# Kernel tuning notes

Measured on AMD Instinct MI355X. Metric: run time of the kernel, lower is better.

The kernel has to match this reference:

```python
import jax, jax.numpy as jnp
import numpy as np

N = 50000        # nodes
E = 800000       # directed edges (before self-loops)
HID = 128
HEADS = 4
LAYERS = 4
D = HID // HEADS  # per-head dim = 32
NEG_SLOPE = 0.2
EPS = 1e-5


def setup_inputs() -> dict:
    key = jax.random.key(0)
    ks = jax.random.split(key, 12)
    s = 0.1
    x = jax.random.normal(ks[0], (N, HID), jnp.float32)
    edge_index = jax.random.randint(ks[1], (2, E), 0, N, jnp.int32)
    # GATv2Conv params per layer: lin_l (source), lin_r (target), att vector, bias
    Wl = s * jax.random.normal(ks[2], (LAYERS, HID, HID), jnp.float32)
    Wr = s * jax.random.normal(ks[3], (LAYERS, HID, HID), jnp.float32)
    att = s * jax.random.normal(ks[4], (LAYERS, HEADS, D), jnp.float32)
    conv_b = jnp.zeros((LAYERS, HID), jnp.float32)
    # GraphNorm params
    gn_w = jnp.ones((LAYERS, HID), jnp.float32)
    gn_b = jnp.zeros((LAYERS, HID), jnp.float32)
    gn_ms = jnp.ones((LAYERS, HID), jnp.float32)  # mean_scale
    # skip projection + final fc
    skip_W = s * jax.random.normal(ks[5], (HID, HID), jnp.float32)
    skip_b = jnp.zeros((HID,), jnp.float32)
    fc_W = s * jax.random.normal(ks[6], (HID, 1), jnp.float32)
    fc_b = jnp.zeros((1,), jnp.float32)
    return {"x": x, "edge_index": edge_index, "Wl": Wl, "Wr": Wr, "att": att,
            "conv_b": conv_b, "gn_w": gn_w, "gn_b": gn_b, "gn_ms": gn_ms,
            "skip_W": skip_W, "skip_b": skip_b, "fc_W": fc_W, "fc_b": fc_b}


def _gatv2_layer(x, src, dst, Wl, Wr, att, bias, n):
    # GATv2Conv: x_l = W_l x_j (messages), x_r = W_r x_i (targets)
    xl = (x @ Wl).reshape(n, HEADS, D)
    xr = (x @ Wr).reshape(n, HEADS, D)
    # edge-wise attention logits: a^T LeakyReLU(x_l[j] + x_r[i])
    e = jax.nn.leaky_relu(xl[src] + xr[dst], NEG_SLOPE)      # [E, H, D]
    score = jnp.einsum('ehd,hd->eh', e, att)                 # [E, H]
    # scatter-softmax over incoming edges of each target node
    smax = jax.ops.segment_max(score, dst, num_segments=n)   # [N, H]
    a = jnp.exp(score - smax[dst])
    denom = jax.ops.segment_sum(a, dst, num_segments=n)
    alpha = a / denom[dst]                                   # [E, H]
    out = jax.ops.segment_sum(alpha[:, :, None] * xl[src], dst, num_segments=n)
    return out.reshape(n, HID) + bias


def _graph_norm(h, w, b, ms):
    # single-graph GraphNorm: x - mean_scale*mean, scaled by per-channel std
    mean = h.mean(axis=0)
    hc = h - ms * mean
    var = (hc * hc).mean(axis=0)
    return w * hc / jnp.sqrt(var + EPS) + b


def reference(x, edge_index, Wl, Wr, att, conv_b, gn_w, gn_b, gn_ms,
              skip_W, skip_b, fc_W, fc_b):
    n = x.shape[0]
    loops = jnp.arange(n, dtype=edge_index.dtype)  # default add_self_loops=True
    src = jnp.concatenate([edge_index[0], loops])
    dst = jnp.concatenate([edge_index[1], loops])
    for l in range(LAYERS):
        h = _gatv2_layer(x, src, dst, Wl[l], Wr[l], att[l], conv_b[l], n)
        h = jax.nn.elu(_graph_norm(h, gn_w[l], gn_b[l], gn_ms[l]))
        x = x + (h @ skip_W + skip_b)  # dropout inactive (eval)
    return (x @ fc_W + fc_b).squeeze(-1)
```

## Files before the change

### kernel.cpp

```cpp
#include <hip/hip_runtime.h>
#include <hip/hip_bf16.h>

#define NN 50000
#define EE 800000
#define NE 850000
#define HID 128
#define NEG_SLOPE 0.2f
#define EPSN 1e-5f
#define NB 196
#define BCAP 6144
#define TB 4096
#define REP 32
#define NPB 16
#define GCAP 768
#define LOG2E 1.4426950408889634f

typedef __attribute__((ext_vector_type(8))) short bf16x8;
typedef __attribute__((ext_vector_type(4))) float f32x4;
typedef __attribute__((ext_vector_type(2))) float f32x2;

__device__ __forceinline__ unsigned short f2b(float f) {
    unsigned u = __float_as_uint(f);
    unsigned r = (u + 0x7FFFu + ((u >> 16) & 1u)) >> 16;
    return (unsigned short)r;
}
__device__ __forceinline__ float b2f(unsigned short u) {
    return __uint_as_float(((unsigned)u) << 16);
}
__device__ __forceinline__ float2 up2(unsigned u) {
    return make_float2(__uint_as_float(u << 16),
                       __uint_as_float(u & 0xFFFF0000u));
}
__device__ __forceinline__ f32x2 up2p(unsigned u) {
    f32x2 r;
    r[0] = __uint_as_float(u << 16);
    r[1] = __uint_as_float(u & 0xFFFF0000u);
    return r;
}
__device__ __forceinline__ f32x2 pka(f32x2 a, f32x2 b) {
    f32x2 d;
    asm("v_pk_add_f32 %0, %1, %2" : "=v"(d) : "v"(a), "v"(b));
    return d;
}
__device__ __forceinline__ f32x2 pkm(f32x2 a, f32x2 b) {
    f32x2 d;
    asm("v_pk_mul_f32 %0, %1, %2" : "=v"(d) : "v"(a), "v"(b));
    return d;
}
__device__ __forceinline__ f32x2 pkf(f32x2 a, f32x2 b, f32x2 c) {
    f32x2 d;
    asm("v_pk_fma_f32 %0, %1, %2, %3" : "=v"(d) : "v"(a), "v"(b), "v"(c));
    return d;
}
__device__ __forceinline__ f32x2 pabs2(f32x2 v) {
    f32x2 r;
    r[0] = __builtin_fabsf(v[0]);
    r[1] = __builtin_fabsf(v[1]);
    return r;
}
#define QPADD(p, CTRL)                                                         \
    __int_as_float(__builtin_amdgcn_update_dpp(                                \
        __float_as_int(p), __float_as_int(p), CTRL, 0xF, 0xF, false))


__global__ void k_prep(const float* __restrict__ x, const float* __restrict__ Wl,
                       const float* __restrict__ Wr, const float* __restrict__ skip_W,
                       unsigned short* __restrict__ xb, unsigned short* __restrict__ wt,
                       unsigned short* __restrict__ st, int* __restrict__ bcnt,
                       float* __restrict__ stats) {
    int i = blockIdx.x * blockDim.x + threadIdx.x;
    if (i < NN * HID / 4) {
        float4 v = *(const float4*)&x[i * 4];
        ushort4 o = {f2b(v.x), f2b(v.y), f2b(v.z), f2b(v.w)};
        *(ushort4*)&xb[i * 4] = o;
    }
    if (i < NB) bcnt[i] = 0;
    if (i < 4 * REP * 256) stats[i] = 0.f;
    if (i < 4 * 256 * 128) {
        int l = i >> 15, idx = i & 32767;
        int j = idx & 7;
        int l16 = (idx >> 3) & 15;
        int quad = (idx >> 7) & 3;
        int ks = (idx >> 9) & 3;
        int ct = idx >> 11;
        int c = ct * 16 + l16;
        int k = quad * 8 + ks * 32 + j;
        float v = (c < 128) ? Wl[l * 16384 + k * 128 + c]
                            : Wr[l * 16384 + k * 128 + (c - 128)];
        wt[i] = f2b(v);
    } else if (i < 4 * 256 * 128 + 128 * 128) {
        int idx = i - 4 * 256 * 128;
        int j = idx & 7;
        int l16 = (idx >> 3) & 15;
        int quad = (idx >> 7) & 3;
        int ks = (idx >> 9) & 3;
        int ct = idx >> 11;
        int c = ct * 16 + l16;
        int k = quad * 8 + ks * 32 + j;
        st[idx] = f2b(skip_W[k * 128 + c]);
    }
}

__global__ void __launch_bounds__(256) k_bin(const int* __restrict__ ei,
                                             int* __restrict__ bcnt,
                                             unsigned* __restrict__ bbuf) {
    __shared__ int hist[NB];
    __shared__ int gbase[NB];
    int t = threadIdx.x;
    for (int b = t; b < NB; b += 256) hist[b] = 0;
    __syncthreads();
    int e0 = blockIdx.x * TB;
    unsigned ent[16];
    int bkt[16];
#pragma unroll
    for (int k = 0; k < 16; k++) {
        int e = e0 + k * 256 + t;
        if (e < NE) {
            int src, dst;
            if (e < EE) { src = ei[e]; dst = ei[EE + e]; }
            else        { src = e - EE; dst = src; }
            int b = dst >> 8;
            ent[k] = ((unsigned)(dst & 255) << 17) | (unsigned)src;
            bkt[k] = b;
            atomicAdd(&hist[b], 1);
        } else bkt[k] = -1;
    }
    __syncthreads();
    for (int b = t; b < NB; b += 256) {
        int c = hist[b];
        gbase[b] = (c > 0) ? atomicAdd(&bcnt[b], c) : 0;
        hist[b] = 0;
    }
    __syncthreads();
#pragma unroll
    for (int k = 0; k < 16; k++) {
        int b = bkt[k];
        if (b >= 0) {
            int pos = gbase[b] + atomicAdd(&hist[b], 1);
            if (pos < BCAP) bbuf[(size_t)b * BCAP + pos] = ent[k];
        }
    }
}

__global__ void __launch_bounds__(256) k_bucket_csr(
    const unsigned* __restrict__ bbuf, const int* __restrict__ bcnt,
    int* __restrict__ row_ptr, int* __restrict__ csr_off) {
    __shared__ unsigned se[BCAP];
    __shared__ int pre[256];
    __shared__ int hist[256], scn[256], exs[256], cur[256];
    int b = blockIdx.x, t = threadIdx.x;
    int bv = (t < NB) ? bcnt[t] : 0;
    pre[t] = bv;
    __syncthreads();
    for (int o = 1; o < 256; o <<= 1) {
        int u = (t >= o) ? pre[t - o] : 0;
        __syncthreads();
        pre[t] += u;
        __syncthreads();
    }
    int cntb = bcnt[b];
    int base = pre[b] - cntb;
    int cnt = min(cntb, BCAP);
    hist[t] = 0;
    cur[t] = 0;
    __syncthreads();
    for (int j = t; j < cnt; j += 256) {
        unsigned e = bbuf[(size_t)b * BCAP + j];
        se[j] = e;
        atomicAdd(&hist[e >> 17], 1);
    }
    __syncthreads();
    int v = hist[t];
    scn[t] = v;
    __syncthreads();
    for (int o = 1; o < 256; o <<= 1) {
        int u = (t >= o) ? scn[t - o] : 0;
        __syncthreads();
        scn[t] += u;
        __syncthreads();
    }
    int ex = scn[t] - v;
    exs[t] = ex;
    int node = b * 256 + t;
    if (node < NN) row_ptr[node] = base + ex;
    if (b == NB - 1 && t == 0) row_ptr[NN] = NE;
    __syncthreads();
    for (int j = t; j < cnt; j += 256) {
        unsigned e = se[j];
        int dl = e >> 17;
        int p = exs[dl] + atomicAdd(&cur[dl], 1);
        csr_off[base + p] = (int)((e & 0x1FFFFu) << 9);
    }
}

__global__ void __launch_bounds__(256) k_gemm_dual_mfma(
    const unsigned short* __restrict__ Xb, const unsigned short* __restrict__ WT,
    unsigned short* __restrict__ C) {
    int w = threadIdx.x >> 6, lane = threadIdx.x & 63;
    int quad = lane >> 4, l16 = lane & 15;
    int r0 = blockIdx.x * 64 + w * 16;
    int lrow = r0 + l16; if (lrow >= NN) lrow = NN - 1;
    const unsigned short* arow = Xb + (size_t)lrow * 128 + quad * 8;
    bf16x8 a[4];
#pragma unroll
    for (int ks = 0; ks < 4; ks++) a[ks] = *(const bf16x8*)(arow + ks * 32);
    const unsigned short* wbase = WT + quad * 128 + l16 * 8;
    f32x4 acc[16];
#pragma unroll
    for (int ct = 0; ct < 16; ct++) acc[ct] = (f32x4){0, 0, 0, 0};
#pragma unroll
    for (int ct = 0; ct < 16; ct++) {
#pragma unroll
        for (int ks = 0; ks < 4; ks++) {
            bf16x8 b = *(const bf16x8*)(wbase + ct * 2048 + ks * 512);
            acc[ct] = __builtin_amdgcn_mfma_f32_16x16x32_bf16(a[ks], b, acc[ct], 0, 0, 0);
        }
    }
    int sr = r0 + quad * 4;
#pragma unroll
    for (int ct = 0; ct < 16; ct++) {
#pragma unroll
        for (int r = 0; r < 4; r++) {
            int rr = sr + r;
            if (rr < NN) C[(size_t)rr * 256 + ct * 16 + l16] = f2b(acc[ct][r]);
        }
    }
}

__device__ __forceinline__ void scoff_reduce(
    const float* __restrict__ stats_l, const float* __restrict__ gn_w,
    const float* __restrict__ gn_b, const float* __restrict__ gn_ms,
    int t, float* s_tot, float* s_sc) {
    float ssum = 0.f;
    const float* sp = stats_l + t;
#pragma unroll
    for (int r = 0; r < REP; r++) ssum += sp[r * 256];
    s_tot[t] = ssum;
    __syncthreads();
    if (t < 128) {
        const float invN = 1.0f / (float)NN;
        float mean = s_tot[t] * invN;
        float ex2 = s_tot[128 + t] * invN;
        float ms = gn_ms[t];
        float var = ex2 - (2.f * ms - ms * ms) * mean * mean;
        float wsc = gn_w[t] * rsqrtf(var + EPSN);
        s_sc[t] = wsc;
        s_sc[128 + t] = gn_b[t] - wsc * ms * mean;
    }
    __syncthreads();
}

__device__ __forceinline__ void skip_core(
    const unsigned short* __restrict__ hbufb, const float* scoff,
    const unsigned short* __restrict__ ST, int lrow, int quad, int l16,
    f32x4 (&acc)[8]) {
    const unsigned short* hrow = hbufb + (size_t)lrow * 128 + quad * 8;
    const unsigned short* stbase = ST + quad * 128 + l16 * 8;
#pragma unroll
    for (int ct = 0; ct < 8; ct++) acc[ct] = (f32x4){0, 0, 0, 0};
#pragma unroll
    for (int ks = 0; ks < 4; ks++) {
        int k0 = ks * 32;
        int kc = quad * 8 + k0;
        uint4 hw = *(const uint4*)(hrow + k0);
        float2 h01 = up2(hw.x), h23 = up2(hw.y), h45 = up2(hw.z), h67 = up2(hw.w);
        float4 sc0 = *(const float4*)(scoff + kc);
        float4 sc1 = *(const float4*)(scoff + kc + 4);
        float4 of0 = *(const float4*)(scoff + 128 + kc);
        float4 of1 = *(const float4*)(scoff + 128 + kc + 4);
        float e[8];
        e[0] = fmaf(sc0.x, h01.x, of0.x); e[1] = fmaf(sc0.y, h01.y, of0.y);
        e[2] = fmaf(sc0.z, h23.x, of0.z); e[3] = fmaf(sc0.w, h23.y, of0.w);
        e[4] = fmaf(sc1.x, h45.x, of1.x); e[5] = fmaf(sc1.y, h45.y, of1.y);
        e[6] = fmaf(sc1.z, h67.x, of1.z); e[7] = fmaf(sc1.w, h67.y, of1.w);
        bf16x8 af;
#pragma unroll
        for (int j = 0; j < 8; j++) {
            float v = e[j];
            v = (v > 0.f) ? v : (__expf(v) - 1.f);
            af[j] = (short)f2b(v);
        }
#pragma unroll
        for (int ct = 0; ct < 8; ct++) {
            bf16x8 b = *(const bf16x8*)(stbase + ct * 2048 + ks * 512);
            acc[ct] = __builtin_amdgcn_mfma_f32_16x16x32_bf16(af, b, acc[ct], 0, 0, 0);
        }
    }
}

__global__ void __launch_bounds__(256) k_skip_dual(
    const unsigned short* __restrict__ hbufb, const float* __restrict__ stats_l,
    const float* __restrict__ gn_w, const float* __restrict__ gn_b,
    const float* __restrict__ gn_ms,
    const unsigned short* __restrict__ ST, const float* __restrict__ skip_b,
    unsigned short* __restrict__ Xb16,
    const unsigned short* __restrict__ WTnext, unsigned short* __restrict__ xlr) {
    __shared__ unsigned short tileX[64][136];
    __shared__ unsigned short tileC[4][16][264];
    __shared__ __align__(16) float s_tot[256];
    __shared__ __align__(16) float s_sc[256];
    int t = threadIdx.x;
    int w = t >> 6, lane = t & 63;
    int quad = lane >> 4, l16 = lane & 15;
    int r0b = blockIdx.x * 64;
    int r0 = r0b + w * 16;
    int lrow = r0 + l16; if (lrow >= NN) lrow = NN - 1;
#pragma unroll
    for (int it = 0; it < 4; it++) {
        int idx = it * 256 + t;
        int row = idx >> 4;
        int c8 = (idx & 15) * 8;
        int rr = r0b + row;
        uint4 v = (rr < NN) ? *(const uint4*)&Xb16[(size_t)rr * 128 + c8]
                            : (uint4){0, 0, 0, 0};
        *(uint4*)&tileX[row][c8] = v;
    }
    scoff_reduce(stats_l, gn_w, gn_b, gn_ms, t, s_tot, s_sc);
    f32x4 acc[8];
    skip_core(hbufb, s_sc, ST, lrow, quad, l16, acc);
    __syncthreads();
#pragma unroll
    for (int ct = 0; ct < 8; ct++) {
        int c = ct * 16 + l16;
        float sb = skip_b[c];
#pragma unroll
        for (int r = 0; r < 4; r++) {
            int wrow = w * 16 + quad * 4 + r;
            float v = b2f(tileX[wrow][c]) + acc[ct][r] + sb;
            tileX[wrow][c] = f2b(v);
        }
    }
    __syncthreads();
#pragma unroll
    for (int it = 0; it < 4; it++) {
        int idx = it * 256 + t;
        int row = idx >> 4;
        int c8 = (idx & 15) * 8;
        int rr = r0b + row;
        if (rr < NN) *(uint4*)&Xb16[(size_t)rr * 128 + c8] = *(const uint4*)&tileX[row][c8];
    }
    int wrowA = w * 16 + l16;
    bf16x8 a[4];
#pragma unroll
    for (int ks = 0; ks < 4; ks++)
        a[ks] = *(const bf16x8*)&tileX[wrowA][quad * 8 + ks * 32];
    const unsigned short* wbase = WTnext + quad * 128 + l16 * 8;
    f32x4 dacc[16];
#pragma unroll
    for (int ct = 0; ct < 16; ct++) dacc[ct] = (f32x4){0, 0, 0, 0};
#pragma unroll
    for (int ct = 0; ct < 16; ct++) {
#pragma unroll
        for (int ks = 0; ks < 4; ks++) {
            bf16x8 b = *(const bf16x8*)(wbase + ct * 2048 + ks * 512);
            dacc[ct] = __builtin_amdgcn_mfma_f32_16x16x32_bf16(a[ks], b, dacc[ct], 0, 0, 0);
        }
    }
#pragma unroll
    for (int ct = 0; ct < 16; ct++) {
#pragma unroll
        for (int r = 0; r < 4; r++)
            tileC[w][quad * 4 + r][ct * 16 + l16] = f2b(dacc[ct][r]);
    }
    __syncthreads();
#pragma unroll
    for (int it = 0; it < 8; it++) {
        int idx = it * 64 + lane;
        int row = idx >> 5;
        int c8 = (idx & 31) * 8;
        int rr = r0 + row;
        if (rr < NN) *(uint4*)&xlr[(size_t)rr * 256 + c8] = *(const uint4*)&tileC[w][row][c8];
    }
}

__global__ void __launch_bounds__(256) k_skip_fc(
    const unsigned short* __restrict__ hbufb, const float* __restrict__ stats_l,
    const float* __restrict__ gn_w, const float* __restrict__ gn_b,
    const float* __restrict__ gn_ms,
    const unsigned short* __restrict__ ST, const float* __restrict__ skip_b,
    const unsigned short* __restrict__ Xb16,
    const float* __restrict__ fc_W, const float* __restrict__ fc_b,
    float* __restrict__ out) {
    __shared__ unsigned short tileX[64][136];
    __shared__ __align__(16) float s_tot[256];
    __shared__ __align__(16) float s_sc[256];
    int t = threadIdx.x;
    int w = t >> 6, lane = t & 63;
    int quad = lane >> 4, l16 = lane & 15;
    int r0b = blockIdx.x * 64;
    int r0 = r0b + w * 16;
    int lrow = r0 + l16; if (lrow >= NN) lrow = NN - 1;
#pragma unroll
    for (int it = 0; it < 4; it++) {
        int idx = it * 256 + t;
        int row = idx >> 4;
        int c8 = (idx & 15) * 8;
        int rr = r0b + row;
        uint4 v = (rr < NN) ? *(const uint4*)&Xb16[(size_t)rr * 128 + c8]
                            : (uint4){0, 0, 0, 0};
        *(uint4*)&tileX[row][c8] = v;
    }
    scoff_reduce(stats_l, gn_w, gn_b, gn_ms, t, s_tot, s_sc);
    f32x4 acc[8];
    skip_core(hbufb, s_sc, ST, lrow, quad, l16, acc);
    __syncthreads();
    float p[4] = {0.f, 0.f, 0.f, 0.f};
#pragma unroll
    for (int ct = 0; ct < 8; ct++) {
        int c = ct * 16 + l16;
        float sb = skip_b[c];
        float fw = fc_W[c];
#pragma unroll
        for (int r = 0; r < 4; r++) {
            int wrow = w * 16 + quad * 4 + r;
            float v = b2f(tileX[wrow][c]) + acc[ct][r] + sb;
            p[r] = fmaf(v, fw, p[r]);
        }
    }
#pragma unroll
    for (int r = 0; r < 4; r++) {
        p[r] += __shfl_xor(p[r], 1);
        p[r] += __shfl_xor(p[r], 2);
        p[r] += __shfl_xor(p[r], 4);
        p[r] += __shfl_xor(p[r], 8);
    }
    if (l16 == 0) {
        float fb = fc_b[0];
#pragma unroll
        for (int r = 0; r < 4; r++) {
            int rr = r0 + quad * 4 + r;
            if (rr < NN) out[rr] = p[r] + fb;
        }
    }
}

__device__ __forceinline__ void proc_edge(
    const uint4& xw, const f32x2* xr2, const f32x2* at06, const f32x2* at04,
    float& den, f32x2* acc) {
    f32x2 f0 = up2p(xw.x), f1 = up2p(xw.y);
    f32x2 f2v = up2p(xw.z), f3 = up2p(xw.w);
    f32x2 s0 = pka(f0, xr2[0]);
    f32x2 s1 = pka(f1, xr2[1]);
    f32x2 s2 = pka(f2v, xr2[2]);
    f32x2 s3 = pka(f3, xr2[3]);
    f32x2 ps1 = pkm(at06[0], s0);
    ps1 = pkf(at04[0], pabs2(s0), ps1);
    ps1 = pkf(at06[1], s1, ps1);
    ps1 = pkf(at04[1], pabs2(s1), ps1);
    f32x2 ps2 = pkm(at06[2], s2);
    ps2 = pkf(at04[2], pabs2(s2), ps2);
    ps2 = pkf(at06[3], s3, ps2);
    ps2 = pkf(at04[3], pabs2(s3), ps2);
    float p = (ps1[0] + ps2[0]) + (ps1[1] + ps2[1]);
    p += QPADD(p, 0xB1);
    p += QPADD(p, 0x4E);
    float w = exp2f(p);
    den += w;
    f32x2 w2; w2[0] = w; w2[1] = w;
    acc[0] = pkf(w2, f0, acc[0]);
    acc[1] = pkf(w2, f1, acc[1]);
    acc[2] = pkf(w2, f2v, acc[2]);
    acc[3] = pkf(w2, f3, acc[3]);
}

__global__ void __launch_bounds__(256) k_gat_node(
    const unsigned short* __restrict__ xlr,
    const float* __restrict__ att, const float* __restrict__ conv_b,
    const int* __restrict__ row_ptr, const int* __restrict__ csr_off,
    unsigned short* __restrict__ houtb, float* __restrict__ stats_l) {
    __shared__ int s_off[GCAP];
    int t = threadIdx.x;
    int wv = t >> 6, lane = t & 63;
    int g = lane >> 4;
    int l = lane & 15;
    int i0 = blockIdx.x * NPB;
    int e0 = row_ptr[i0];
    int cnt = row_ptr[i0 + NPB] - e0;
    int stged = min(cnt, GCAP);
    for (int k = t; k < stged; k += 256) s_off[k] = csr_off[e0 + k];
    int n0 = i0 + wv * 4;
    int rp[5];
#pragma unroll
    for (int k = 0; k <= 4; k++) rp[k] = row_ptr[n0 + k];
    __syncthreads();

    const char* xbytes = (const char*)xlr;
    int lofs = 16 * l;
    f32x2 at06[4], at04[4];
    {
        float4 a0 = *(const float4*)&att[8 * l];
        float4 a1 = *(const float4*)&att[8 * l + 4];
        const float c6 = 0.6f * LOG2E, c4 = 0.4f * LOG2E;
        at06[0][0] = a0.x * c6; at06[0][1] = a0.y * c6;
        at06[1][0] = a0.z * c6; at06[1][1] = a0.w * c6;
        at06[2][0] = a1.x * c6; at06[2][1] = a1.y * c6;
        at06[3][0] = a1.z * c6; at06[3][1] = a1.w * c6;
        at04[0][0] = a0.x * c4; at04[0][1] = a0.y * c4;
        at04[1][0] = a0.z * c4; at04[1][1] = a0.w * c4;
        at04[2][0] = a1.x * c4; at04[2][1] = a1.y * c4;
        at04[3][0] = a1.z * c4; at04[3][1] = a1.w * c4;
    }
    int c0p = 8 * l + 2 * g;
    float2 cbp = *(const float2*)&conv_b[c0p];
    float saA = 0.f, sqA = 0.f, saB = 0.f, sqB = 0.f;

    uint4 xr_raw = *(const uint4*)(xbytes + (size_t)n0 * 512 + 256 + lofs);
    int start = rp[0] - e0, end = rp[1] - e0;
    int j = start + g;
    bool vA = j < end;
    bool vB = (j + 4) < end;
    bool vC = false;
    uint4 xwA = {0, 0, 0, 0}, xwB = {0, 0, 0, 0}, xwC = {0, 0, 0, 0};
    if (vA) { int o = (j < stged) ? s_off[j] : csr_off[e0 + j];
              xwA = *(const uint4*)(xbytes + (size_t)(unsigned)o + lofs); }
    if (vB) { int o = (j + 4 < stged) ? s_off[j + 4] : csr_off[e0 + j + 4];
              xwB = *(const uint4*)(xbytes + (size_t)(unsigned)o + lofs); }

    for (int nn = 0; nn < 4; nn++) {
        f32x2 xr2[4];
        xr2[0] = up2p(xr_raw.x); xr2[1] = up2p(xr_raw.y);
        xr2[2] = up2p(xr_raw.z); xr2[3] = up2p(xr_raw.w);
        float den = 0.f;
        f32x2 acc[4];
#pragma unroll
        for (int k = 0; k < 4; k++) { acc[k][0] = 0.f; acc[k][1] = 0.f; }
        for (;;) {
            if (!vA) break;
            {
                bool vn = (j + 8) < end;
                if (vn) { int o = (j + 8 < stged) ? s_off[j + 8] : csr_off[e0 + j + 8];
                          xwC = *(const uint4*)(xbytes + (size_t)(unsigned)o + lofs); }
                vC = vn;
                proc_edge(xwA, xr2, at06, at04, den, acc);
                j += 4;
            }
            if (!vB) break;
            {
                bool vn = (j + 8) < end;
                if (vn) { int o = (j + 8 < stged) ? s_off[j + 8] : csr_off[e0 + j + 8];
                          xwA = *(const uint4*)(xbytes + (size_t)(unsigned)o + lofs); }
                vA = vn;
                proc_edge(xwB, xr2, at06, at04, den, acc);
                j += 4;
            }
            if (!vC) break;
            {
                bool vn = (j + 8) < end;
                if (vn) { int o = (j + 8 < stged) ? s_off[j + 8] : csr_off[e0 + j + 8];
                          xwB = *(const uint4*)(xbytes + (size_t)(unsigned)o + lofs); }
                vB = vn;
                proc_edge(xwC, xr2, at06, at04, den, acc);
                j += 4;
            }
        }
        float r0v = acc[0][0], r1v = acc[0][1], r2v = acc[1][0], r3v = acc[1][1];
        float r4v = acc[2][0], r5v = acc[2][1], r6v = acc[3][0], r7v = acc[3][1];
        float dn = den;
        if (nn < 3) {
            xr_raw = *(const uint4*)(xbytes + (size_t)(n0 + nn + 1) * 512 + 256 + lofs);
            start = rp[nn + 1] - e0; end = rp[nn + 2] - e0;
            j = start + g;
            vA = j < end;
            vB = (j + 4) < end;
            xwA = (uint4){0, 0, 0, 0}; xwB = (uint4){0, 0, 0, 0};
            if (vA) { int o = (j < stged) ? s_off[j] : csr_off[e0 + j];
                      xwA = *(const uint4*)(xbytes + (size_t)(unsigned)o + lofs); }
            if (vB) { int o = (j + 4 < stged) ? s_off[j + 4] : csr_off[e0 + j + 4];
                      xwB = *(const uint4*)(xbytes + (size_t)(unsigned)o + lofs); }
        }
        r0v += __shfl_xor(r0v, 16); r0v += __shfl_xor(r0v, 32);
        r1v += __shfl_xor(r1v, 16); r1v += __shfl_xor(r1v, 32);
        r2v += __shfl_xor(r2v, 16); r2v += __shfl_xor(r2v, 32);
        r3v += __shfl_xor(r3v, 16); r3v += __shfl_xor(r3v, 32);
        r4v += __shfl_xor(r4v, 16); r4v += __shfl_xor(r4v, 32);
        r5v += __shfl_xor(r5v, 16); r5v += __shfl_xor(r5v, 32);
        r6v += __shfl_xor(r6v, 16); r6v += __shfl_xor(r6v, 32);
        r7v += __shfl_xor(r7v, 16); r7v += __shfl_xor(r7v, 32);
        dn  += __shfl_xor(dn, 16);  dn  += __shfl_xor(dn, 32);
        float rA = (g == 0) ? r0v : (g == 1) ? r2v : (g == 2) ? r4v : r6v;
        float rB = (g == 0) ? r1v : (g == 1) ? r3v : (g == 2) ? r5v : r7v;
        float invd = 1.0f / dn;
        float hA = fmaf(rA, invd, cbp.x);
        float hB = fmaf(rB, invd, cbp.y);
        unsigned pkv = (unsigned)f2b(hA) | ((unsigned)f2b(hB) << 16);
        *(unsigned*)&houtb[(size_t)(n0 + nn) * 128 + c0p] = pkv;
        saA += hA; sqA += hA * hA;
        saB += hB; sqB += hB * hB;
    }
    {
        float* srep = stats_l + (size_t)(blockIdx.x & (REP - 1)) * 256;
        atomicAdd(&srep[c0p], saA);
        atomicAdd(&srep[c0p + 1], saB);
        atomicAdd(&srep[128 + c0p], sqA);
        atomicAdd(&srep[128 + c0p + 1], sqB);
    }
}

extern "C" void kernel_launch(void* const* d_in, const int* in_sizes, int n_in,
                              void* d_out, int out_size, void* d_ws, size_t ws_size,
                              hipStream_t stream) {
    const float* x_in   = (const float*)d_in[0];
    const int*   ei     = (const int*)d_in[1];
    const float* Wl     = (const float*)d_in[2];
    const float* Wr     = (const float*)d_in[3];
    const float* att    = (const float*)d_in[4];
    const float* conv_b = (const float*)d_in[5];
    const float* gn_w   = (const float*)d_in[6];
    const float* gn_b   = (const float*)d_in[7];
    const float* gn_ms  = (const float*)d_in[8];
    const float* skip_W = (const float*)d_in[9];
    const float* skip_b = (const float*)d_in[10];
    const float* fc_W   = (const float*)d_in[11];
    const float* fc_b   = (const float*)d_in[12];
    float* out = (float*)d_out;

    float* ws = (float*)d_ws;
    float* stats = ws;
    unsigned short* xlr   = (unsigned short*)(stats + 4 * REP * 256);
    unsigned short* b16X  = xlr + (size_t)NN * 256;
    unsigned short* hbufb = b16X + NN * HID;
    unsigned short* wt    = hbufb + NN * HID;
    unsigned short* st    = wt + 4 * 256 * 128;
    int* row_ptr = (int*)(st + 128 * 128);
    int* bcnt    = row_ptr + NN + 1;
    int* csr_off = bcnt + NB;
    unsigned* bbuf = (unsigned*)(csr_off + NE);

    k_prep<<<(NN * HID / 4 + 255) / 256, 256, 0, stream>>>(
        x_in, Wl, Wr, skip_W, b16X, wt, st, bcnt, stats);

    k_bin<<<(NE + TB - 1) / TB, 256, 0, stream>>>(ei, bcnt, bbuf);
    k_bucket_csr<<<NB, 256, 0, stream>>>(bbuf, bcnt, row_ptr, csr_off);

    const int rtiles = (NN + 63) / 64;
    const int gat_blocks = NN / NPB;
    k_gemm_dual_mfma<<<rtiles, 256, 0, stream>>>(b16X, wt, xlr);
    for (int l = 0; l < 4; l++) {
        float* stats_l = stats + (size_t)l * REP * 256;
        k_gat_node<<<gat_blocks, 256, 0, stream>>>(
            xlr, att + l * HID, conv_b + l * HID, row_ptr, csr_off,
            hbufb, stats_l);
        if (l < 3) {
            k_skip_dual<<<rtiles, 256, 0, stream>>>(
                hbufb, stats_l, gn_w + l * HID, gn_b + l * HID, gn_ms + l * HID,
                st, skip_b, b16X, wt + (size_t)(l + 1) * 256 * 128, xlr);
        } else {
            k_skip_fc<<<rtiles, 256, 0, stream>>>(
                hbufb, stats_l, gn_w + l * HID, gn_b + l * HID, gn_ms + l * HID,
                st, skip_b, b16X, fc_W, fc_b, out);
        }
    }
}
```

Before: 467.0 us.

## Halve GAT node block size and deepen edge gather prefetch to three

The GAT aggregation kernel now uses 128-thread blocks covering 8 nodes instead of 256 threads covering 16, with a smaller shared offset staging buffer. The manually unrolled two-ahead gather pipeline becomes a rotating three-deep prefetch loop, so more neighbor loads are in flight per lane. Smaller blocks aim to balance load across uneven node degrees. The deeper rotation may cost registers and occupancy, and the 8-node block setting has to stay consistent with the per-block stats layout.

Measured after the change: 436.3 us, median of 2. 6.6% less time.

```diff
diff --git a/kernel.cpp b/kernel.cpp
--- a/kernel.cpp
+++ b/kernel.cpp
@@ -11,8 +11,8 @@
 #define BCAP 6144
 #define TB 4096
 #define REP 32
-#define NPB 16
-#define GCAP 768
+#define NPB 8
+#define GCAP 512
 #define LOG2E 1.4426950408889634f
 
 typedef __attribute__((ext_vector_type(8))) short bf16x8;
@@ -463,7 +463,7 @@
     acc[3] = pkf(w2, f3, acc[3]);
 }
 
-__global__ void __launch_bounds__(256) k_gat_node(
+__global__ void __launch_bounds__(128) k_gat_node(
     const unsigned short* __restrict__ xlr,
     const float* __restrict__ att, const float* __restrict__ conv_b,
     const int* __restrict__ row_ptr, const int* __restrict__ csr_off,
@@ -477,7 +477,7 @@
     int e0 = row_ptr[i0];
     int cnt = row_ptr[i0 + NPB] - e0;
     int stged = min(cnt, GCAP);
-    for (int k = t; k < stged; k += 256) s_off[k] = csr_off[e0 + k];
+    for (int k = t; k < stged; k += 128) s_off[k] = csr_off[e0 + k];
     int n0 = i0 + wv * 4;
     int rp[5];
 #pragma unroll
@@ -507,14 +507,16 @@
     uint4 xr_raw = *(const uint4*)(xbytes + (size_t)n0 * 512 + 256 + lofs);
     int start = rp[0] - e0, end = rp[1] - e0;
     int j = start + g;
-    bool vA = j < end;
-    bool vB = (j + 4) < end;
-    bool vC = false;
-    uint4 xwA = {0, 0, 0, 0}, xwB = {0, 0, 0, 0}, xwC = {0, 0, 0, 0};
-    if (vA) { int o = (j < stged) ? s_off[j] : csr_off[e0 + j];
-              xwA = *(const uint4*)(xbytes + (size_t)(unsigned)o + lofs); }
-    if (vB) { int o = (j + 4 < stged) ? s_off[j + 4] : csr_off[e0 + j + 4];
-              xwB = *(const uint4*)(xbytes + (size_t)(unsigned)o + lofs); }
+    bool v0 = j < end;
+    bool v1 = (j + 4) < end;
+    bool v2 = (j + 8) < end;
+    uint4 xw0 = {0, 0, 0, 0}, xw1 = {0, 0, 0, 0}, xw2 = {0, 0, 0, 0};
+    if (v0) { int o = (j < stged) ? s_off[j] : csr_off[e0 + j];
+              xw0 = *(const uint4*)(xbytes + (size_t)(unsigned)o + lofs); }
+    if (v1) { int o = (j + 4 < stged) ? s_off[j + 4] : csr_off[e0 + j + 4];
+              xw1 = *(const uint4*)(xbytes + (size_t)(unsigned)o + lofs); }
+    if (v2) { int o = (j + 8 < stged) ? s_off[j + 8] : csr_off[e0 + j + 8];
+              xw2 = *(const uint4*)(xbytes + (size_t)(unsigned)o + lofs); }
 
     for (int nn = 0; nn < 4; nn++) {
         f32x2 xr2[4];
@@ -524,34 +526,15 @@
         f32x2 acc[4];
 #pragma unroll
         for (int k = 0; k < 4; k++) { acc[k][0] = 0.f; acc[k][1] = 0.f; }
-        for (;;) {
-            if (!vA) break;
-            {
-                bool vn = (j + 8) < end;
-                if (vn) { int o = (j + 8 < stged) ? s_off[j + 8] : csr_off[e0 + j + 8];
-                          xwC = *(const uint4*)(xbytes + (size_t)(unsigned)o + lofs); }
-                vC = vn;
-                proc_edge(xwA, xr2, at06, at04, den, acc);
-                j += 4;
-            }
-            if (!vB) break;
-            {
-                bool vn = (j + 8) < end;
-                if (vn) { int o = (j + 8 < stged) ? s_off[j + 8] : csr_off[e0 + j + 8];
-                          xwA = *(const uint4*)(xbytes + (size_t)(unsigned)o + lofs); }
-                vA = vn;
-                proc_edge(xwB, xr2, at06, at04, den, acc);
-                j += 4;
-            }
-            if (!vC) break;
-            {
-                bool vn = (j + 8) < end;
-                if (vn) { int o = (j + 8 < stged) ? s_off[j + 8] : csr_off[e0 + j + 8];
-                          xwB = *(const uint4*)(xbytes + (size_t)(unsigned)o + lofs); }
-                vB = vn;
-                proc_edge(xwC, xr2, at06, at04, den, acc);
-                j += 4;
-            }
+        while (v0) {
+            bool v3 = (j + 12) < end;
+            uint4 xw3 = {0, 0, 0, 0};
+            if (v3) { int o = (j + 12 < stged) ? s_off[j + 12] : csr_off[e0 + j + 12];
+                      xw3 = *(const uint4*)(xbytes + (size_t)(unsigned)o + lofs); }
+            proc_edge(xw0, xr2, at06, at04, den, acc);
+            j += 4;
+            v0 = v1; v1 = v2; v2 = v3;
+            xw0 = xw1; xw1 = xw2; xw2 = xw3;
         }
         float r0v = acc[0][0], r1v = acc[0][1], r2v = acc[1][0], r3v = acc[1][1];
         float r4v = acc[2][0], r5v = acc[2][1], r6v = acc[3][0], r7v = acc[3][1];
@@ -560,13 +543,17 @@
             xr_raw = *(const uint4*)(xbytes + (size_t)(n0 + nn + 1) * 512 + 256 + lofs);
             start = rp[nn + 1] - e0; end = rp[nn + 2] - e0;
             j = start + g;
-            vA = j < end;
-            vB = (j + 4) < end;
-            xwA = (uint4){0, 0, 0, 0}; xwB = (uint4){0, 0, 0, 0};
-            if (vA) { int o = (j < stged) ? s_off[j] : csr_off[e0 + j];
-                      xwA = *(const uint4*)(xbytes + (size_t)(unsigned)o + lofs); }
-            if (vB) { int o = (j + 4 < stged) ? s_off[j + 4] : csr_off[e0 + j + 4];
-                      xwB = *(const uint4*)(xbytes + (size_t)(unsigned)o + lofs); }
+            v0 = j < end;
+            v1 = (j + 4) < end;
+            v2 = (j + 8) < end;
+            xw0 = (uint4){0, 0, 0, 0}; xw1 = (uint4){0, 0, 0, 0};
+            xw2 = (uint4){0, 0, 0, 0};
+            if (v0) { int o = (j < stged) ? s_off[j] : csr_off[e0 + j];
+                      xw0 = *(const uint4*)(xbytes + (size_t)(unsigned)o + lofs); }
+            if (v1) { int o = (j + 4 < stged) ? s_off[j + 4] : csr_off[e0 + j + 4];
+                      xw1 = *(const uint4*)(xbytes + (size_t)(unsigned)o + lofs); }
+            if (v2) { int o = (j + 8 < stged) ? s_off[j + 8] : csr_off[e0 + j + 8];
+                      xw2 = *(const uint4*)(xbytes + (size_t)(unsigned)o + lofs); }
         }
         r0v += __shfl_xor(r0v, 16); r0v += __shfl_xor(r0v, 32);
         r1v += __shfl_xor(r1v, 16); r1v += __shfl_xor(r1v, 32);
@@ -633,11 +620,11 @@
     k_bucket_csr<<<NB, 256, 0, stream>>>(bbuf, bcnt, row_ptr, csr_off);
 
     const int rtiles = (NN + 63) / 64;
-    const int gat_blocks = NN / NPB;
+    const int gat_blocks = (NN + NPB - 1) / NPB;
     k_gemm_dual_mfma<<<rtiles, 256, 0, stream>>>(b16X, wt, xlr);
     for (int l = 0; l < 4; l++) {
         float* stats_l = stats + (size_t)l * REP * 256;
-        k_gat_node<<<gat_blocks, 256, 0, stream>>>(
+        k_gat_node<<<gat_blocks, 128, 0, stream>>>(
             xlr, att + l * HID, conv_b + l * HID, row_ptr, csr_off,
             hbufb, stats_l);
         if (l < 3) {
```

## Halve GAT node block size and reduce edge-prefetch ring from three to two buffers

Applied to the files above, without the earlier changes.

The GAT aggregation kernel now runs 128-thread blocks covering 8 nodes each, and the LDS staging for edge offsets shrinks to 512 entries. The three-buffer rotating edge prefetch becomes a two-buffer scheme: each gathered row is unpacked into registers before its buffer is refilled with the load two edges ahead. The aim is lower register and LDS pressure per block, for higher occupancy and better tail balance across the many small blocks. The cost is a shallower prefetch distance, so fewer gathers are in flight per wave.

Measured after the change: 449.1 us. -3.8%, faster.

```diff
diff --git a/kernel.cpp b/kernel.cpp
--- a/kernel.cpp
+++ b/kernel.cpp
@@ -11,8 +11,8 @@
 #define BCAP 6144
 #define TB 4096
 #define REP 32
-#define NPB 16
-#define GCAP 768
+#define NPB 8
+#define GCAP 512
 #define LOG2E 1.4426950408889634f
 
 typedef __attribute__((ext_vector_type(8))) short bf16x8;
@@ -434,11 +434,10 @@
     }
 }
 
-__device__ __forceinline__ void proc_edge(
-    const uint4& xw, const f32x2* xr2, const f32x2* at06, const f32x2* at04,
+__device__ __forceinline__ void score_accum(
+    f32x2 f0, f32x2 f1, f32x2 f2v, f32x2 f3,
+    const f32x2* xr2, const f32x2* at06, const f32x2* at04,
     float& den, f32x2* acc) {
-    f32x2 f0 = up2p(xw.x), f1 = up2p(xw.y);
-    f32x2 f2v = up2p(xw.z), f3 = up2p(xw.w);
     f32x2 s0 = pka(f0, xr2[0]);
     f32x2 s1 = pka(f1, xr2[1]);
     f32x2 s2 = pka(f2v, xr2[2]);
@@ -463,7 +462,7 @@
     acc[3] = pkf(w2, f3, acc[3]);
 }
 
-__global__ void __launch_bounds__(256) k_gat_node(
+__global__ void __launch_bounds__(128) k_gat_node(
     const unsigned short* __restrict__ xlr,
     const float* __restrict__ att, const float* __restrict__ conv_b,
     const int* __restrict__ row_ptr, const int* __restrict__ csr_off,
@@ -477,7 +476,7 @@
     int e0 = row_ptr[i0];
     int cnt = row_ptr[i0 + NPB] - e0;
     int stged = min(cnt, GCAP);
-    for (int k = t; k < stged; k += 256) s_off[k] = csr_off[e0 + k];
+    for (int k = t; k < stged; k += 128) s_off[k] = csr_off[e0 + k];
     int n0 = i0 + wv * 4;
     int rp[5];
 #pragma unroll
@@ -509,8 +508,7 @@
     int j = start + g;
     bool vA = j < end;
     bool vB = (j + 4) < end;
-    bool vC = false;
-    uint4 xwA = {0, 0, 0, 0}, xwB = {0, 0, 0, 0}, xwC = {0, 0, 0, 0};
+    uint4 xwA = {0, 0, 0, 0}, xwB = {0, 0, 0, 0};
     if (vA) { int o = (j < stged) ? s_off[j] : csr_off[e0 + j];
               xwA = *(const uint4*)(xbytes + (size_t)(unsigned)o + lofs); }
     if (vB) { int o = (j + 4 < stged) ? s_off[j + 4] : csr_off[e0 + j + 4];
@@ -524,32 +522,26 @@
         f32x2 acc[4];
 #pragma unroll
         for (int k = 0; k < 4; k++) { acc[k][0] = 0.f; acc[k][1] = 0.f; }
-        for (;;) {
-            if (!vA) break;
+        while (vA) {
             {
+                f32x2 f0 = up2p(xwA.x), f1 = up2p(xwA.y);
+                f32x2 f2v = up2p(xwA.z), f3 = up2p(xwA.w);
                 bool vn = (j + 8) < end;
                 if (vn) { int o = (j + 8 < stged) ? s_off[j + 8] : csr_off[e0 + j + 8];
-                          xwC = *(const uint4*)(xbytes + (size_t)(unsigned)o + lofs); }
-                vC = vn;
-                proc_edge(xwA, xr2, at06, at04, den, acc);
+                          xwA = *(const uint4*)(xbytes + (size_t)(unsigned)o + lofs); }
+                vA = vn;
+                score_accum(f0, f1, f2v, f3, xr2, at06, at04, den, acc);
                 j += 4;
             }
             if (!vB) break;
             {
-                bool vn = (j + 8) < end;
-                if (vn) { int o = (j + 8 < stged) ? s_off[j + 8] : csr_off[e0 + j + 8];
-                          xwA = *(const uint4*)(xbytes + (size_t)(unsigned)o + lofs); }
-                vA = vn;
-                proc_edge(xwB, xr2, at06, at04, den, acc);
-                j += 4;
-            }
-            if (!vC) break;
-            {
+                f32x2 f0 = up2p(xwB.x), f1 = up2p(xwB.y);
+                f32x2 f2v = up2p(xwB.z), f3 = up2p(xwB.w);
                 bool vn = (j + 8) < end;
                 if (vn) { int o = (j + 8 < stged) ? s_off[j + 8] : csr_off[e0 + j + 8];
                           xwB = *(const uint4*)(xbytes + (size_t)(unsigned)o + lofs); }
                 vB = vn;
-                proc_edge(xwC, xr2, at06, at04, den, acc);
+                score_accum(f0, f1, f2v, f3, xr2, at06, at04, den, acc);
                 j += 4;
             }
         }
@@ -633,11 +625,11 @@
     k_bucket_csr<<<NB, 256, 0, stream>>>(bbuf, bcnt, row_ptr, csr_off);
 
     const int rtiles = (NN + 63) / 64;
-    const int gat_blocks = NN / NPB;
+    const int gat_blocks = (NN + NPB - 1) / NPB;
     k_gemm_dual_mfma<<<rtiles, 256, 0, stream>>>(b16X, wt, xlr);
     for (int l = 0; l < 4; l++) {
         float* stats_l = stats + (size_t)l * REP * 256;
-        k_gat_node<<<gat_blocks, 256, 0, stream>>>(
+        k_gat_node<<<gat_blocks, 128, 0, stream>>>(
             xlr, att + l * HID, conv_b + l * HID, row_ptr, csr_off,
             hbufb, stats_l);
         if (l < 3) {
```
